# Kernel optimization log

Measured on AMD Instinct MI355X. Metric: run time of the kernel, lower is better.

The kernel has to match this reference:

```python
import jax, jax.numpy as jnp
import numpy as np

ITERATIONS = 20


def _affine_sample(canvas, theta):
    """PyTorch-equivalent F.affine_grid + F.grid_sample (bilinear,
    align_corners=False, padding_mode='zeros') for all T transforms at once.
    canvas: [H, W], theta: [T, 2, 3] -> returns [T, H, W].
    """
    H, W = canvas.shape
    dt = canvas.dtype
    # Normalized base grid coords, align_corners=False: centers of pixels.
    xs = (jnp.arange(W, dtype=dt) * 2 + 1) / W - 1  # [W]
    ys = (jnp.arange(H, dtype=dt) * 2 + 1) / H - 1  # [H]
    # Sampled normalized coords: [x', y'] = theta @ [x, y, 1]
    gx = (theta[:, 0, 0, None, None] * xs[None, None, :]
          + theta[:, 0, 1, None, None] * ys[None, :, None]
          + theta[:, 0, 2, None, None])  # [T, H, W]
    gy = (theta[:, 1, 0, None, None] * xs[None, None, :]
          + theta[:, 1, 1, None, None] * ys[None, :, None]
          + theta[:, 1, 2, None, None])  # [T, H, W]
    # Unnormalize to pixel coords (align_corners=False).
    ix = (gx + 1) * (W * 0.5) - 0.5
    iy = (gy + 1) * (H * 0.5) - 0.5
    x0f = jnp.floor(ix)
    y0f = jnp.floor(iy)
    wx1 = ix - x0f
    wy1 = iy - y0f
    wx0 = 1 - wx1
    wy0 = 1 - wy1
    x0 = x0f.astype(jnp.int32)
    y0 = y0f.astype(jnp.int32)

    def corner(xi, yi):
        valid = (xi >= 0) & (xi < W) & (yi >= 0) & (yi < H)
        v = canvas[jnp.clip(yi, 0, H - 1), jnp.clip(xi, 0, W - 1)]
        return jnp.where(valid, v, jnp.zeros((), dt))  # zeros padding

    return (wx0 * wy0 * corner(x0, y0)
            + wx1 * wy0 * corner(x0 + 1, y0)
            + wx0 * wy1 * corner(x0, y0 + 1)
            + wx1 * wy1 * corner(x0 + 1, y0 + 1))


def setup_inputs() -> dict:
    key = jax.random.key(0)
    k1, k2, k3 = jax.random.split(key, 3)
    H, W, T = 1024, 1024, 16
    canvas0 = jax.random.uniform(k1, (H, W), dtype=jnp.float32)
    theta = jax.random.normal(k2, (T, 2, 3), dtype=jnp.float32)
    probs = jax.random.uniform(k3, (T,), dtype=jnp.float32)
    base_value = jnp.zeros((1,), dtype=jnp.float32)
    return {"canvas0": canvas0, "theta": theta, "probs": probs,
            "base_value": base_value}


def reference(canvas0, theta, probs, base_value):
    p = probs / jnp.sum(probs)

    def step(canvas, _):
        sampled = _affine_sample(canvas, theta)          # [T, H, W]
        new_canvas = jnp.einsum('t,thw->hw', p, sampled)  # weighted IFS sum
        return new_canvas, None

    canvas, _ = jax.lax.scan(step, canvas0, None, length=ITERATIONS)
    return canvas + base_value[0]
```

## Files before the change

kernel.cpp:

```cpp
#include <hip/hip_runtime.h>

constexpr int W = 1024;
constexpr int H = 1024;
constexpr int T = 16;
constexpr int ITERS = 20;
constexpr int PITCH = 1040;
constexpr int PH = H + 2;
constexpr int PAD_ELEMS = PH * PITCH;
constexpr int TILES_X = W / 16;
constexpr int TILES_Y = H / 16;

__global__ void setup_coef(const float* __restrict__ theta,
                           const float* __restrict__ probs,
                           float* __restrict__ coef) {
    int t = threadIdx.x;
    if (t >= T) return;
    float sum = 0.f;
    for (int i = 0; i < T; ++i) sum += probs[i];
    float p = probs[t] / sum;
    const float* th = theta + 6 * t;
    float a = th[0], b = th[1], c = th[2];
    float d = th[3], e = th[4], f = th[5];
    float Cx = a * ((1.0f - (float)W) * 0.5f)
             + b * ((1.0f - (float)H) * 0.5f)
             + (c + 1.0f) * ((float)W * 0.5f) - 0.5f;
    float Cy = d * ((1.0f - (float)W) * 0.5f)
             + e * ((1.0f - (float)H) * 0.5f)
             + (f + 1.0f) * ((float)H * 0.5f) - 0.5f;
    float* o = coef + 8 * t;
    o[0] = p;  o[1] = a;  o[2] = b;  o[3] = Cx + 1.0f;
    o[4] = d;  o[5] = e;  o[6] = Cy + 1.0f; o[7] = 0.f;
}

__global__ __launch_bounds__(256) void setup_mask(const float* __restrict__ coef,
                                                  unsigned* __restrict__ mask) {
    int tile = blockIdx.x * 256 + threadIdx.x;
    if (tile >= TILES_X * TILES_Y) return;
    int tx = tile & (TILES_X - 1), ty = tile / TILES_X;
    float w0 = (float)(tx * 16), w1 = w0 + 15.f;
    float h0 = (float)(ty * 16), h1 = h0 + 15.f;
    unsigned m = 0;
    for (int t = 0; t < T; ++t) {
        float Ax = coef[t * 8 + 1], Bx = coef[t * 8 + 2], Cx = coef[t * 8 + 3];
        float Ay = coef[t * 8 + 4], By = coef[t * 8 + 5], Cy = coef[t * 8 + 6];
        float ixmin = Cx + (Ax >= 0.f ? Ax * w0 : Ax * w1) + (Bx >= 0.f ? Bx * h0 : Bx * h1);
        float ixmax = Cx + (Ax >= 0.f ? Ax * w1 : Ax * w0) + (Bx >= 0.f ? Bx * h1 : Bx * h0);
        float iymin = Cy + (Ay >= 0.f ? Ay * w0 : Ay * w1) + (By >= 0.f ? By * h0 : By * h1);
        float iymax = Cy + (Ay >= 0.f ? Ay * w1 : Ay * w0) + (By >= 0.f ? By * h1 : By * h0);
        bool hit = !(ixmax <= 0.f || ixmin >= (float)(W + 1) ||
                     iymax <= 0.f || iymin >= (float)(H + 1));
        if (hit) m |= (1u << t);
    }
    mask[tile] = m;
}

__global__ __launch_bounds__(256) void copy_in(const float* __restrict__ src,
                                               float* __restrict__ dst) {
    int i = blockIdx.x * 256 + threadIdx.x;
    int h = i >> 10, w = i & 1023;
    dst[(h + 1) * PITCH + (w + 1)] = src[i];
}

__global__ __launch_bounds__(256) void ifs_iter(const float* __restrict__ in,
                                                float* __restrict__ out,
                                                const float* __restrict__ coef,
                                                const unsigned* __restrict__ mask,
                                                const float* __restrict__ base,
                                                int dstPitch, int dstOff,
                                                int add_base) {
    __shared__ float sc[T * 8];
    if (threadIdx.x < T * 8) sc[threadIdx.x] = coef[threadIdx.x];
    __syncthreads();

    unsigned tmask = mask[blockIdx.y * TILES_X + blockIdx.x];

    int lane = threadIdx.x & 63;
    int wv   = threadIdx.x >> 6;
    int w = blockIdx.x * 16 + ((wv & 1) << 3) + (lane & 7);
    int h = blockIdx.y * 16 + ((wv >> 1) << 3) + (lane >> 3);
    float wf = (float)w, hf = (float)h;

    float acc = 0.f;

#pragma unroll
    for (int g = 0; g < T / 2; ++g) {
        if (((tmask >> (2 * g)) & 3u) == 0u) continue;

        const float* c0 = sc + 16 * g;
        const float* c1 = sc + 16 * g + 8;
        float p0 = c0[0], Ax0 = c0[1], Bx0 = c0[2], Cx0 = c0[3];
        float Ay0 = c0[4], By0 = c0[5], Cy0 = c0[6];
        float p1 = c1[0], Ax1 = c1[1], Bx1 = c1[2], Cx1 = c1[3];
        float Ay1 = c1[4], By1 = c1[5], Cy1 = c1[6];

        float ix0 = fmaf(Ax0, wf, fmaf(Bx0, hf, Cx0));
        float iy0 = fmaf(Ay0, wf, fmaf(By0, hf, Cy0));
        float ix1 = fmaf(Ax1, wf, fmaf(Bx1, hf, Cx1));
        float iy1 = fmaf(Ay1, wf, fmaf(By1, hf, Cy1));
        float xf0 = floorf(ix0), yf0 = floorf(iy0);
        float xf1 = floorf(ix1), yf1 = floorf(iy1);
        bool act0 = (xf0 >= 0.f) & (xf0 <= (float)W) & (yf0 >= 0.f) & (yf0 <= (float)H);
        bool act1 = (xf1 >= 0.f) & (xf1 <= (float)W) & (yf1 >= 0.f) & (yf1 <= (float)H);
        int idx0 = act0 ? (int)fmaf(yf0, (float)PITCH, xf0) : 0;
        int idx1 = act1 ? (int)fmaf(yf1, (float)PITCH, xf1) : 0;
        float pe0 = act0 ? p0 : 0.f;
        float pe1 = act1 ? p1 : 0.f;

        const float* q0 = in + idx0;
        const float* q1 = in + idx1;
        float a00 = q0[0], a01 = q0[1], a10 = q0[PITCH], a11 = q0[PITCH + 1];
        float b00 = q1[0], b01 = q1[1], b10 = q1[PITCH], b11 = q1[PITCH + 1];

        float fx0 = ix0 - xf0, fy0 = iy0 - yf0;
        float fx1 = ix1 - xf1, fy1 = iy1 - yf1;
        float ta = fmaf(fx0, a01 - a00, a00);
        float ua = fmaf(fx0, a11 - a10, a10);
        float va = fmaf(fy0, ua - ta, ta);
        float tb = fmaf(fx1, b01 - b00, b00);
        float ub = fmaf(fx1, b11 - b10, b10);
        float vb = fmaf(fy1, ub - tb, tb);
        acc = fmaf(pe0, va, fmaf(pe1, vb, acc));
    }

    if (add_base) acc += base[0];
    out[h * dstPitch + w + dstOff] = acc;
}

extern "C" void kernel_launch(void* const* d_in, const int* in_sizes, int n_in,
                              void* d_out, int out_size, void* d_ws, size_t ws_size,
                              hipStream_t stream) {
    const float* canvas0 = (const float*)d_in[0];
    const float* theta   = (const float*)d_in[1];
    const float* probs   = (const float*)d_in[2];
    const float* base    = (const float*)d_in[3];
    float* out = (float*)d_out;

    float* bufA = (float*)d_ws;
    float* bufB = bufA + PAD_ELEMS;
    float* coef = bufB + PAD_ELEMS;
    unsigned* mask = (unsigned*)(coef + T * 8);

    hipMemsetAsync(d_ws, 0, (size_t)2 * PAD_ELEMS * sizeof(float), stream);

    setup_coef<<<1, 64, 0, stream>>>(theta, probs, coef);
    setup_mask<<<(TILES_X * TILES_Y + 255) / 256, 256, 0, stream>>>(coef, mask);
    copy_in<<<(H * W) / 256, 256, 0, stream>>>(canvas0, bufA);

    dim3 block(256);
    dim3 grid(TILES_X, TILES_Y);

    const float* cur = bufA;
    for (int i = 0; i < ITERS; ++i) {
        bool last = (i == ITERS - 1);
        float* dst = last ? out : ((i & 1) ? bufA : bufB);
        int dstPitch = last ? W : PITCH;
        int dstOff   = last ? 0 : (PITCH + 1);
        ifs_iter<<<grid, block, 0, stream>>>(cur, dst, coef, mask, base,
                                             dstPitch, dstOff, last ? 1 : 0);
        cur = dst;
    }
}
```

Baseline: 444.3 us.

## Compact active transforms per tile and batch four gathers with paired loads

Each block now packs the coefficients of only the transforms whose mask bit is set into shared memory, with zero padding, and loops over the active count in groups of four. Each group issues all of its address computations, then all of its 2-wide vector loads (each covering the two horizontally adjacent texels in a row), then the blends. This removes the pairwise mask skipping that wasted half of each pair, halves the number of load instructions, and raises memory-level parallelism. The cost is a runtime-bounded loop in place of a fully unrolled one, with up to three padded zero-weight transforms per group, and the 2-wide loads may be unaligned.

```diff
diff --git a/kernel.cpp b/kernel.cpp
--- a/kernel.cpp
+++ b/kernel.cpp
@@ -9,6 +9,8 @@
 constexpr int PAD_ELEMS = PH * PITCH;
 constexpr int TILES_X = W / 16;
 constexpr int TILES_Y = H / 16;
+
+typedef float f2 __attribute__((ext_vector_type(2), aligned(4)));
 
 __global__ void setup_coef(const float* __restrict__ theta,
                            const float* __restrict__ probs,
@@ -68,58 +70,60 @@
                                                 const float* __restrict__ base,
                                                 int dstPitch, int dstOff,
                                                 int add_base) {
-    __shared__ float sc[T * 8];
-    if (threadIdx.x < T * 8) sc[threadIdx.x] = coef[threadIdx.x];
+    __shared__ float sc[(T + 3) * 8];
+
+    unsigned tmask = mask[blockIdx.y * TILES_X + blockIdx.x];
+    int nact = __popc(tmask);
+    int lid = threadIdx.x;
+
+    if (lid < T * 8) {
+        int t = lid >> 3;
+        if (tmask & (1u << t)) {
+            int pos = __popc(tmask & ((1u << t) - 1));
+            sc[pos * 8 + (lid & 7)] = coef[lid];
+        }
+    }
+    if (lid < 24) sc[nact * 8 + lid] = 0.f;
     __syncthreads();
 
-    unsigned tmask = mask[blockIdx.y * TILES_X + blockIdx.x];
-
-    int lane = threadIdx.x & 63;
-    int wv   = threadIdx.x >> 6;
+    int lane = lid & 63;
+    int wv   = lid >> 6;
     int w = blockIdx.x * 16 + ((wv & 1) << 3) + (lane & 7);
     int h = blockIdx.y * 16 + ((wv >> 1) << 3) + (lane >> 3);
     float wf = (float)w, hf = (float)h;
 
     float acc = 0.f;
 
+    for (int g = 0; g < nact; g += 4) {
+        const float* c = sc + g * 8;
+        float fx[4], fy[4], pe[4];
+        int id0[4];
 #pragma unroll
-    for (int g = 0; g < T / 2; ++g) {
-        if (((tmask >> (2 * g)) & 3u) == 0u) continue;
-
-        const float* c0 = sc + 16 * g;
-        const float* c1 = sc + 16 * g + 8;
-        float p0 = c0[0], Ax0 = c0[1], Bx0 = c0[2], Cx0 = c0[3];
-        float Ay0 = c0[4], By0 = c0[5], Cy0 = c0[6];
-        float p1 = c1[0], Ax1 = c1[1], Bx1 = c1[2], Cx1 = c1[3];
-        float Ay1 = c1[4], By1 = c1[5], Cy1 = c1[6];
-
-        float ix0 = fmaf(Ax0, wf, fmaf(Bx0, hf, Cx0));
-        float iy0 = fmaf(Ay0, wf, fmaf(By0, hf, Cy0));
-        float ix1 = fmaf(Ax1, wf, fmaf(Bx1, hf, Cx1));
-        float iy1 = fmaf(Ay1, wf, fmaf(By1, hf, Cy1));
-        float xf0 = floorf(ix0), yf0 = floorf(iy0);
-        float xf1 = floorf(ix1), yf1 = floorf(iy1);
-        bool act0 = (xf0 >= 0.f) & (xf0 <= (float)W) & (yf0 >= 0.f) & (yf0 <= (float)H);
-        bool act1 = (xf1 >= 0.f) & (xf1 <= (float)W) & (yf1 >= 0.f) & (yf1 <= (float)H);
-        int idx0 = act0 ? (int)fmaf(yf0, (float)PITCH, xf0) : 0;
-        int idx1 = act1 ? (int)fmaf(yf1, (float)PITCH, xf1) : 0;
-        float pe0 = act0 ? p0 : 0.f;
-        float pe1 = act1 ? p1 : 0.f;
-
-        const float* q0 = in + idx0;
-        const float* q1 = in + idx1;
-        float a00 = q0[0], a01 = q0[1], a10 = q0[PITCH], a11 = q0[PITCH + 1];
-        float b00 = q1[0], b01 = q1[1], b10 = q1[PITCH], b11 = q1[PITCH + 1];
-
-        float fx0 = ix0 - xf0, fy0 = iy0 - yf0;
-        float fx1 = ix1 - xf1, fy1 = iy1 - yf1;
-        float ta = fmaf(fx0, a01 - a00, a00);
-        float ua = fmaf(fx0, a11 - a10, a10);
-        float va = fmaf(fy0, ua - ta, ta);
-        float tb = fmaf(fx1, b01 - b00, b00);
-        float ub = fmaf(fx1, b11 - b10, b10);
-        float vb = fmaf(fy1, ub - tb, tb);
-        acc = fmaf(pe0, va, fmaf(pe1, vb, acc));
+        for (int k = 0; k < 4; ++k) {
+            const float* ck = c + k * 8;
+            float p = ck[0], Ax = ck[1], Bx = ck[2], Cx = ck[3];
+            float Ay = ck[4], By = ck[5], Cy = ck[6];
+            float x = fmaf(Ax, wf, fmaf(Bx, hf, Cx));
+            float y = fmaf(Ay, wf, fmaf(By, hf, Cy));
+            float xf = floorf(x), yf = floorf(y);
+            bool act = (xf >= 0.f) & (xf <= (float)W) & (yf >= 0.f) & (yf <= (float)H);
+            id0[k] = act ? (int)fmaf(yf, (float)PITCH, xf) : 0;
+            pe[k]  = act ? p : 0.f;
+            fx[k] = x - xf;
+            fy[k] = y - yf;
+        }
+        f2 r0[4], r1[4];
+#pragma unroll
+        for (int k = 0; k < 4; ++k) {
+            r0[k] = *(const f2*)(in + id0[k]);
+            r1[k] = *(const f2*)(in + id0[k] + PITCH);
+        }
+#pragma unroll
+        for (int k = 0; k < 4; ++k) {
+            float top = fmaf(fx[k], r0[k].y - r0[k].x, r0[k].x);
+            float bot = fmaf(fx[k], r1[k].y - r1[k].x, r1[k].x);
+            acc = fmaf(pe[k], fmaf(fy[k], bot - top, top), acc);
+        }
     }
 
     if (add_base) acc += base[0];
```

Result: faster. 416.4 us (-6.3%).
